# Kernel optimization log

Hardware: AMD Instinct MI355X
Metric: run time of the kernel (lower is better)

Reference implementation:

```python
import jax, jax.numpy as jnp
import numpy as np

B, S, D = 8, 1024, 1024
H = 2048            # expert hidden dim
E = 8               # num experts
TOP_K = 2
D_NOISE = 256
TEMP = 1.0


def setup_inputs() -> dict:
    key = jax.random.key(0)
    ks = jax.random.split(key, 8)
    return {
        "x": jax.random.normal(ks[0], (B, S, D), dtype=jnp.float32),
        "noise_clock_emb": jax.random.normal(ks[1], (B, D_NOISE), dtype=jnp.float32),
        # router weight [D_noise, E] (xavier-ish scale)
        "route_weight": jax.random.normal(ks[2], (D_NOISE, E), dtype=jnp.float32) * (1.0 / np.sqrt(D_NOISE)),
        # stacked expert params; torch Linear y = x @ W.T + b, stored here pre-transposed
        "fc_in_w": jax.random.normal(ks[3], (E, D, 2 * H), dtype=jnp.float32) * 0.02,
        "fc_in_b": jax.random.normal(ks[4], (E, 2 * H), dtype=jnp.float32) * 0.02,
        "fc_out_w": jax.random.normal(ks[5], (E, H, D), dtype=jnp.float32) * 0.02,
        "fc_out_b": jax.random.normal(ks[6], (E, D), dtype=jnp.float32) * 0.02,
    }


def reference(x, noise_clock_emb, route_weight, fc_in_w, fc_in_b, fc_out_w, fc_out_b):
    # ---- router: P = softmax(phi(sigma) @ W_R / T) ----
    logits = (noise_clock_emb @ route_weight) / TEMP            # [B, E]
    probs = jax.nn.softmax(logits, axis=-1)
    topk_weights, topk_indices = jax.lax.top_k(probs, TOP_K)    # [B, K]
    topk_weights = topk_weights / jnp.clip(
        topk_weights.sum(axis=-1, keepdims=True), 1e-8)
    # dense per-(batch, expert) mixing coefficient, identical to the
    # masked accumulation in the torch loop
    coeff = jnp.einsum("bke,bk->be",
                       jax.nn.one_hot(topk_indices, E, dtype=x.dtype),
                       topk_weights)                             # [B, E]

    # ---- all experts densely over the full batch (matches original math) ----
    h = jnp.einsum("bsd,edh->ebsh", x, fc_in_w) + fc_in_b[:, None, None, :]
    value, gate = jnp.split(h, 2, axis=-1)                       # [E,B,S,H] each
    hidden = value * jax.nn.silu(gate)
    mixed = jnp.einsum("ebsh,ehd,be->bsd", hidden, fc_out_w, coeff)
    mixed = mixed + jnp.einsum("be,ed->bd", coeff, fc_out_b)[:, None, :]
    return mixed, logits, probs, topk_indices, topk_weights
```

## Files before the change

kernel.cpp:

```cpp
#include <hip/hip_runtime.h>
#include <stdint.h>

#define B_ 8
#define S_ 1024
#define D_ 1024
#define H_ 2048
#define E_ 8
#define DN_ 256

typedef unsigned char u8;
typedef float f32x4 __attribute__((ext_vector_type(4)));
typedef long long ll;

__device__ __forceinline__ u8 f2f8(float f) {
  return (u8)(__builtin_amdgcn_cvt_pk_fp8_f32(f, f, 0, false) & 0xff);
}
__device__ __forceinline__ unsigned int pk4f8(float a, float b, float c, float d) {
  int w = __builtin_amdgcn_cvt_pk_fp8_f32(a, b, 0, false);
  w = __builtin_amdgcn_cvt_pk_fp8_f32(c, d, w, true);
  return (unsigned int)w;
}

__device__ __forceinline__ void gll16(const void* g, void* l) {
  __builtin_amdgcn_global_load_lds(
      (__attribute__((address_space(1))) void*)g,
      (__attribute__((address_space(3))) void*)l, 16, 0, 0);
}

__device__ __forceinline__ int swz(int r) { return (r & 3) ^ ((r >> 2) & 1); }

__global__ void router_kernel(const float* __restrict__ noise,
                              const float* __restrict__ rw,
                              float* __restrict__ out_logits,
                              float* __restrict__ out_probs,
                              float* __restrict__ out_idx,
                              float* __restrict__ out_w,
                              int* __restrict__ ws_idx,
                              float* __restrict__ ws_w) {
  __shared__ float sl[64];
  __shared__ float sp[64];
  const int t = threadIdx.x;
  const int b = t >> 3, e = t & 7;
  float acc = 0.f;
  for (int d = 0; d < DN_; ++d) acc += noise[b * DN_ + d] * rw[d * E_ + e];
  sl[t] = acc;
  out_logits[t] = acc;
  __syncthreads();
  float m = -1e30f;
  for (int j = 0; j < 8; ++j) m = fmaxf(m, sl[b * 8 + j]);
  float s = 0.f;
  for (int j = 0; j < 8; ++j) s += __expf(sl[b * 8 + j] - m);
  const float p = __expf(acc - m) / s;
  out_probs[t] = p;
  sp[t] = p;
  __syncthreads();
  if (e == 0) {
    int a1 = 0; float v1 = sp[b * 8];
    for (int j = 1; j < 8; ++j) { float v = sp[b * 8 + j]; if (v > v1) { v1 = v; a1 = j; } }
    int a2 = -1; float v2 = -1e30f;
    for (int j = 0; j < 8; ++j) {
      if (j == a1) continue;
      float v = sp[b * 8 + j]; if (v > v2) { v2 = v; a2 = j; }
    }
    float sum = fmaxf(v1 + v2, 1e-8f);
    float w1 = v1 / sum, w2 = v2 / sum;
    out_idx[b * 2] = (float)a1; out_idx[b * 2 + 1] = (float)a2;
    out_w[b * 2] = w1; out_w[b * 2 + 1] = w2;
    ws_idx[b * 2] = a1; ws_idx[b * 2 + 1] = a2;
    ws_w[b * 2] = w1; ws_w[b * 2 + 1] = w2;
  }
}

__global__ void cast_x_kernel(const float* __restrict__ x, unsigned int* __restrict__ xq) {
  const size_t i = (size_t)blockIdx.x * blockDim.x + threadIdx.x;
  float4 v = *(const float4*)(x + i * 4);
  xq[i] = pk4f8(v.x, v.y, v.z, v.w);
}

template <int R, int C>
__global__ void transpose_cast_kernel(const float* __restrict__ in, u8* __restrict__ out) {
  __shared__ u8 tile[64][72];
  const int e = blockIdx.z;
  const float* ip = in + (size_t)e * R * C;
  u8* op = out + (size_t)e * R * C;
  const int r0 = blockIdx.y * 64, c0 = blockIdx.x * 64;
  const int t = threadIdx.x;
  const int rr = t >> 4;
  const int c4 = t & 15;
#pragma unroll
  for (int i = 0; i < 4; ++i) {
    const int r = rr + i * 16;
    float4 v = *(const float4*)(ip + (size_t)(r0 + r) * C + c0 + c4 * 4);
    tile[c4 * 4 + 0][r] = f2f8(v.x);
    tile[c4 * 4 + 1][r] = f2f8(v.y);
    tile[c4 * 4 + 2][r] = f2f8(v.z);
    tile[c4 * 4 + 3][r] = f2f8(v.w);
  }
  __syncthreads();
#pragma unroll
  for (int i = 0; i < 4; ++i) {
    const int c = rr + i * 16;
    unsigned int w = *(const unsigned int*)&tile[c][c4 * 4];
    *(unsigned int*)(op + (size_t)(c0 + c) * R + r0 + c4 * 4) = w;
  }
}

__global__ void __launch_bounds__(256, 4) gemm1_kernel(
    const u8* __restrict__ xq,
    const u8* __restrict__ wtin,
    const float* __restrict__ bin,
    const int* __restrict__ ws_idx, const float* __restrict__ ws_w,
    u8* __restrict__ hid)
{
  const int nt = blockIdx.x;
  const int mt = blockIdx.y;
  const int z  = blockIdx.z;
  const int b  = z >> 1;
  const int e  = ws_idx[z] & 7;
  const float csc = ws_w[z];

  __shared__ u8 As[128 * 64];
  __shared__ u8 Bs[128 * 64];

  const int t = threadIdx.x;
  const int wave = t >> 6, lane = t & 63;
  const int wm = wave >> 1, wn = wave & 1;
  const int lm = lane & 15, lq = lane >> 4;
  const int lrow4 = lane >> 2;
  const int kq = ((lane & 3) ^ swz(lrow4)) * 16;
  const int fsw = swz(lm);
  const int p0 = lq >> 1, fb = (lq & 1) * 8;

  const u8* Ab  = xq + (size_t)b * (S_ * D_) + (size_t)mt * 128 * D_;
  const u8* Bvb = wtin + (size_t)e * (2 * H_ * D_) + (size_t)nt * 64 * D_;
  const u8* Bgb = Bvb + (size_t)H_ * D_;

  const f32x4 vz = {0.f, 0.f, 0.f, 0.f};
  f32x4 accv[4][2], accg[4][2];
#pragma unroll
  for (int i = 0; i < 4; ++i)
#pragma unroll
    for (int j = 0; j < 2; ++j) { accv[i][j] = vz; accg[i][j] = vz; }

  for (int kt = 0; kt < D_ / 64; ++kt) {
    const int k0 = kt * 64 + kq;
    gll16(Ab + (size_t)(wave * 16 + lrow4) * D_ + k0, (char*)As + wave * 1024);
    gll16(Ab + (size_t)((wave + 4) * 16 + lrow4) * D_ + k0, (char*)As + (wave + 4) * 1024);
    gll16(Bvb + (size_t)(wave * 16 + lrow4) * D_ + k0, (char*)Bs + wave * 1024);
    gll16(Bgb + (size_t)(wave * 16 + lrow4) * D_ + k0, (char*)Bs + 4096 + wave * 1024);
    __syncthreads();
    ll af[4][2], bvf[2][2], bgf[2][2];
#pragma unroll
    for (int h = 0; h < 2; ++h) {
      const int pw = ((h * 2 + p0) ^ fsw) * 16 + fb;
#pragma unroll
      for (int i = 0; i < 4; ++i)
        af[i][h] = *(const ll*)(As + (wm * 64 + i * 16 + lm) * 64 + pw);
#pragma unroll
      for (int j = 0; j < 2; ++j) {
        bvf[j][h] = *(const ll*)(Bs + (wn * 32 + j * 16 + lm) * 64 + pw);
        bgf[j][h] = *(const ll*)(Bs + (64 + wn * 32 + j * 16 + lm) * 64 + pw);
      }
    }
#pragma unroll
    for (int h = 0; h < 2; ++h)
#pragma unroll
      for (int i = 0; i < 4; ++i)
#pragma unroll
        for (int j = 0; j < 2; ++j) {
          accv[i][j] = __builtin_amdgcn_mfma_f32_16x16x32_fp8_fp8(af[i][h], bvf[j][h], accv[i][j], 0, 0, 0);
          accg[i][j] = __builtin_amdgcn_mfma_f32_16x16x32_fp8_fp8(af[i][h], bgf[j][h], accg[i][j], 0, 0, 0);
        }
    __syncthreads();
  }

  u8* hb = hid + (size_t)z * (S_ * H_);
  const int row0 = mt * 128 + wm * 64;
  const int col0 = nt * 64 + wn * 32;
#pragma unroll
  for (int j = 0; j < 2; ++j) {
    const int col = col0 + j * 16 + lm;
    const float bvx = bin[e * 2 * H_ + col];
    const float bgx = bin[e * 2 * H_ + H_ + col];
#pragma unroll
    for (int i = 0; i < 4; ++i) {
#pragma unroll
      for (int r = 0; r < 4; ++r) {
        const int srow = row0 + i * 16 + lq * 4 + r;
        float v = accv[i][j][r] + bvx;
        float g = accg[i][j][r] + bgx;
        float hv = v * g / (1.f + __expf(-g)) * csc;
        hb[(size_t)srow * H_ + col] = f2f8(hv);
      }
    }
  }
}

__global__ void __launch_bounds__(256, 2) gemm2_kernel(
    const u8* __restrict__ hid,
    const u8* __restrict__ wtout,
    const float* __restrict__ bout,
    const int* __restrict__ ws_idx, const float* __restrict__ ws_w,
    float* __restrict__ out)
{
  const int nt = blockIdx.x;
  const int mt = blockIdx.y;
  const int b  = blockIdx.z;

  __shared__ u8 As[128 * 64];
  __shared__ u8 Bs[128 * 64];

  const int t = threadIdx.x;
  const int wave = t >> 6, lane = t & 63;
  const int wm = wave >> 1, wn = wave & 1;
  const int lm = lane & 15, lq = lane >> 4;
  const int lrow4 = lane >> 2;
  const int kq = ((lane & 3) ^ swz(lrow4)) * 16;
  const int fsw = swz(lm);
  const int p0 = lq >> 1, fb = (lq & 1) * 8;

  const f32x4 vz = {0.f, 0.f, 0.f, 0.f};
  f32x4 acc[4][4];
#pragma unroll
  for (int i = 0; i < 4; ++i)
#pragma unroll
    for (int j = 0; j < 4; ++j) acc[i][j] = vz;

  for (int slot = 0; slot < 2; ++slot) {
    const int e = ws_idx[b * 2 + slot] & 7;
    const u8* Ab = hid + ((size_t)(b * 2 + slot) * S_ + mt * 128) * H_;
    const u8* Bb = wtout + ((size_t)e * D_ + nt * 128) * H_;
    for (int kt = 0; kt < H_ / 64; ++kt) {
      const int k0 = kt * 64 + kq;
      gll16(Ab + (size_t)(wave * 16 + lrow4) * H_ + k0, (char*)As + wave * 1024);
      gll16(Ab + (size_t)((wave + 4) * 16 + lrow4) * H_ + k0, (char*)As + (wave + 4) * 1024);
      gll16(Bb + (size_t)(wave * 16 + lrow4) * H_ + k0, (char*)Bs + wave * 1024);
      gll16(Bb + (size_t)((wave + 4) * 16 + lrow4) * H_ + k0, (char*)Bs + (wave + 4) * 1024);
      __syncthreads();
      ll af[4][2], bf[4][2];
#pragma unroll
      for (int h = 0; h < 2; ++h) {
        const int pw = ((h * 2 + p0) ^ fsw) * 16 + fb;
#pragma unroll
        for (int i = 0; i < 4; ++i)
          af[i][h] = *(const ll*)(As + (wm * 64 + i * 16 + lm) * 64 + pw);
#pragma unroll
        for (int j = 0; j < 4; ++j)
          bf[j][h] = *(const ll*)(Bs + (wn * 64 + j * 16 + lm) * 64 + pw);
      }
#pragma unroll
      for (int h = 0; h < 2; ++h)
#pragma unroll
        for (int i = 0; i < 4; ++i)
#pragma unroll
          for (int j = 0; j < 4; ++j)
            acc[i][j] = __builtin_amdgcn_mfma_f32_16x16x32_fp8_fp8(af[i][h], bf[j][h], acc[i][j], 0, 0, 0);
      __syncthreads();
    }
  }

  const int e0 = ws_idx[b * 2] & 7, e1 = ws_idx[b * 2 + 1] & 7;
  const float c0 = ws_w[b * 2], c1 = ws_w[b * 2 + 1];
  float* ob = out + (size_t)b * (S_ * D_);
  const int row0 = mt * 128 + wm * 64;
  const int col0 = nt * 128 + wn * 64;
#pragma unroll
  for (int j = 0; j < 4; ++j) {
    const int col = col0 + j * 16 + lm;
    const float bias = c0 * bout[e0 * D_ + col] + c1 * bout[e1 * D_ + col];
#pragma unroll
    for (int i = 0; i < 4; ++i)
#pragma unroll
      for (int r = 0; r < 4; ++r)
        ob[(size_t)(row0 + i * 16 + lq * 4 + r) * D_ + col] = acc[i][j][r] + bias;
  }
}

extern "C" void kernel_launch(void* const* d_in, const int* in_sizes, int n_in,
                              void* d_out, int out_size, void* d_ws, size_t ws_size,
                              hipStream_t stream) {
  const float* x     = (const float*)d_in[0];
  const float* noise = (const float*)d_in[1];
  const float* rw    = (const float*)d_in[2];
  const float* fiw   = (const float*)d_in[3];
  const float* fib   = (const float*)d_in[4];
  const float* fow   = (const float*)d_in[5];
  const float* fob   = (const float*)d_in[6];
  float* out = (float*)d_out;

  char* ws = (char*)d_ws;
  int*   ws_idx = (int*)ws;
  float* ws_w   = (float*)(ws + 64);
  u8* xq    = (u8*)(ws + 256);
  u8* wtin  = xq + (size_t)B_ * S_ * D_;
  u8* wtout = wtin + (size_t)E_ * 2 * H_ * D_;
  u8* hid   = wtout + (size_t)E_ * D_ * H_;

  float* out_mixed  = out;
  float* out_logits = out + (size_t)B_ * S_ * D_;
  float* out_probs  = out_logits + B_ * E_;
  float* out_idx    = out_probs + B_ * E_;
  float* out_w      = out_idx + B_ * 2;

  router_kernel<<<1, 64, 0, stream>>>(noise, rw, out_logits, out_probs,
                                      out_idx, out_w, ws_idx, ws_w);
  cast_x_kernel<<<(B_ * S_ * D_ / 4) / 256, 256, 0, stream>>>(x, (unsigned int*)xq);
  transpose_cast_kernel<D_, 2 * H_><<<dim3((2 * H_) / 64, D_ / 64, E_), 256, 0, stream>>>(fiw, wtin);
  transpose_cast_kernel<H_, D_><<<dim3(D_ / 64, H_ / 64, E_), 256, 0, stream>>>(fow, wtout);
  gemm1_kernel<<<dim3(32, 8, 16), 256, 0, stream>>>(xq, wtin, fib, ws_idx, ws_w, hid);
  gemm2_kernel<<<dim3(8, 8, 8), 256, 0, stream>>>(hid, wtout, fob, ws_idx, ws_w, out_mixed);
}
```

Baseline: 464.0 us.

## Merge router, casts and transposes into one prep kernel; halve gemm2 N tile

Folds the router, the x fp8 cast and both weight transpose-casts into a single block-indexed prep kernel, removing three launches and the gaps between them. The router now splits its dot product across four lanes with shuffle reduction. Separately, gemm2 moves to a 128x64 tile with twice as many blocks and higher launch-bounds occupancy, so more of the GPU is busy in that stage. The trade-off is that the A tile is loaded twice as often in gemm2, and the router block runs alongside the bulk cast blocks.

Result: faster. 432.0 us (-6.9%).

```diff
diff --git a/kernel.cpp b/kernel.cpp
--- a/kernel.cpp
+++ b/kernel.cpp
@@ -29,62 +29,12 @@
 
 __device__ __forceinline__ int swz(int r) { return (r & 3) ^ ((r >> 2) & 1); }
 
-__global__ void router_kernel(const float* __restrict__ noise,
-                              const float* __restrict__ rw,
-                              float* __restrict__ out_logits,
-                              float* __restrict__ out_probs,
-                              float* __restrict__ out_idx,
-                              float* __restrict__ out_w,
-                              int* __restrict__ ws_idx,
-                              float* __restrict__ ws_w) {
-  __shared__ float sl[64];
-  __shared__ float sp[64];
-  const int t = threadIdx.x;
-  const int b = t >> 3, e = t & 7;
-  float acc = 0.f;
-  for (int d = 0; d < DN_; ++d) acc += noise[b * DN_ + d] * rw[d * E_ + e];
-  sl[t] = acc;
-  out_logits[t] = acc;
-  __syncthreads();
-  float m = -1e30f;
-  for (int j = 0; j < 8; ++j) m = fmaxf(m, sl[b * 8 + j]);
-  float s = 0.f;
-  for (int j = 0; j < 8; ++j) s += __expf(sl[b * 8 + j] - m);
-  const float p = __expf(acc - m) / s;
-  out_probs[t] = p;
-  sp[t] = p;
-  __syncthreads();
-  if (e == 0) {
-    int a1 = 0; float v1 = sp[b * 8];
-    for (int j = 1; j < 8; ++j) { float v = sp[b * 8 + j]; if (v > v1) { v1 = v; a1 = j; } }
-    int a2 = -1; float v2 = -1e30f;
-    for (int j = 0; j < 8; ++j) {
-      if (j == a1) continue;
-      float v = sp[b * 8 + j]; if (v > v2) { v2 = v; a2 = j; }
-    }
-    float sum = fmaxf(v1 + v2, 1e-8f);
-    float w1 = v1 / sum, w2 = v2 / sum;
-    out_idx[b * 2] = (float)a1; out_idx[b * 2 + 1] = (float)a2;
-    out_w[b * 2] = w1; out_w[b * 2 + 1] = w2;
-    ws_idx[b * 2] = a1; ws_idx[b * 2 + 1] = a2;
-    ws_w[b * 2] = w1; ws_w[b * 2 + 1] = w2;
-  }
-}
-
-__global__ void cast_x_kernel(const float* __restrict__ x, unsigned int* __restrict__ xq) {
-  const size_t i = (size_t)blockIdx.x * blockDim.x + threadIdx.x;
-  float4 v = *(const float4*)(x + i * 4);
-  xq[i] = pk4f8(v.x, v.y, v.z, v.w);
-}
-
 template <int R, int C>
-__global__ void transpose_cast_kernel(const float* __restrict__ in, u8* __restrict__ out) {
-  __shared__ u8 tile[64][72];
-  const int e = blockIdx.z;
-  const float* ip = in + (size_t)e * R * C;
-  u8* op = out + (size_t)e * R * C;
-  const int r0 = blockIdx.y * 64, c0 = blockIdx.x * 64;
-  const int t = threadIdx.x;
+__device__ __forceinline__ void transpose_body(const float* __restrict__ ip,
+                                               u8* __restrict__ op,
+                                               int bx, int by, int t,
+                                               u8 (&tile)[64][72]) {
+  const int r0 = by * 64, c0 = bx * 64;
   const int rr = t >> 4;
   const int c4 = t & 15;
 #pragma unroll
@@ -102,6 +52,91 @@
     const int c = rr + i * 16;
     unsigned int w = *(const unsigned int*)&tile[c][c4 * 4];
     *(unsigned int*)(op + (size_t)(c0 + c) * R + r0 + c4 * 4) = w;
+  }
+}
+
+#define NCAST (B_ * S_ * D_ / 1024)
+#define NT1 ((2 * H_ / 64) * (D_ / 64) * E_)
+#define NT2 ((D_ / 64) * (H_ / 64) * E_)
+
+__global__ void __launch_bounds__(256) prep_kernel(
+    const float* __restrict__ x, const float* __restrict__ noise,
+    const float* __restrict__ rw, const float* __restrict__ fiw,
+    const float* __restrict__ fow,
+    float* __restrict__ out_logits, float* __restrict__ out_probs,
+    float* __restrict__ out_idx, float* __restrict__ out_w,
+    int* __restrict__ ws_idx, float* __restrict__ ws_w,
+    unsigned int* __restrict__ xq, u8* __restrict__ wtin,
+    u8* __restrict__ wtout) {
+  __shared__ __align__(16) u8 tile[64][72];
+  const int t = threadIdx.x;
+  int bid = blockIdx.x;
+
+  if (bid == 0) {
+    float* sl = (float*)&tile[0][0];
+    float* sp = sl + 64;
+    {
+      const int pair = t >> 2, sub = t & 3;
+      const int b = pair >> 3, e = pair & 7;
+      float acc = 0.f;
+      const int d0 = sub * 64;
+      for (int d = d0; d < d0 + 64; ++d)
+        acc += noise[b * DN_ + d] * rw[d * E_ + e];
+      acc += __shfl_xor(acc, 1);
+      acc += __shfl_xor(acc, 2);
+      if (sub == 0) sl[pair] = acc;
+    }
+    __syncthreads();
+    if (t < 64) {
+      const int b = t >> 3;
+      float L = sl[t];
+      out_logits[t] = L;
+      float m = -1e30f;
+      for (int j = 0; j < 8; ++j) m = fmaxf(m, sl[b * 8 + j]);
+      float s = 0.f;
+      for (int j = 0; j < 8; ++j) s += __expf(sl[b * 8 + j] - m);
+      float p = __expf(L - m) / s;
+      out_probs[t] = p;
+      sp[t] = p;
+    }
+    __syncthreads();
+    if (t < 64 && (t & 7) == 0) {
+      const int b = t >> 3;
+      int a1 = 0; float v1 = sp[b * 8];
+      for (int j = 1; j < 8; ++j) { float v = sp[b * 8 + j]; if (v > v1) { v1 = v; a1 = j; } }
+      int a2 = -1; float v2 = -1e30f;
+      for (int j = 0; j < 8; ++j) {
+        if (j == a1) continue;
+        float v = sp[b * 8 + j]; if (v > v2) { v2 = v; a2 = j; }
+      }
+      float sum = fmaxf(v1 + v2, 1e-8f);
+      float w1 = v1 / sum, w2 = v2 / sum;
+      out_idx[b * 2] = (float)a1; out_idx[b * 2 + 1] = (float)a2;
+      out_w[b * 2] = w1; out_w[b * 2 + 1] = w2;
+      ws_idx[b * 2] = a1; ws_idx[b * 2 + 1] = a2;
+      ws_w[b * 2] = w1; ws_w[b * 2 + 1] = w2;
+    }
+    return;
+  }
+  bid -= 1;
+  if (bid < NCAST) {
+    const size_t i = (size_t)bid * 256 + t;
+    float4 v = *((const float4*)x + i);
+    xq[i] = pk4f8(v.x, v.y, v.z, v.w);
+    return;
+  }
+  bid -= NCAST;
+  if (bid < NT1) {
+    const int bx = bid & 63, by = (bid >> 6) & 15, e = bid >> 10;
+    transpose_body<D_, 2 * H_>(fiw + (size_t)e * D_ * 2 * H_,
+                               wtin + (size_t)e * D_ * 2 * H_, bx, by, t, tile);
+    return;
+  }
+  bid -= NT1;
+  {
+    const int bx = bid & 15, by = (bid >> 4) & 31, e = bid >> 9;
+    transpose_body<H_, D_>(fow + (size_t)e * H_ * D_,
+                           wtout + (size_t)e * H_ * D_, bx, by, t, tile);
   }
 }
 
@@ -196,7 +231,7 @@
   }
 }
 
-__global__ void __launch_bounds__(256, 2) gemm2_kernel(
+__global__ void __launch_bounds__(256, 4) gemm2_kernel(
     const u8* __restrict__ hid,
     const u8* __restrict__ wtout,
     const float* __restrict__ bout,
@@ -208,7 +243,7 @@
   const int b  = blockIdx.z;
 
   __shared__ u8 As[128 * 64];
-  __shared__ u8 Bs[128 * 64];
+  __shared__ u8 Bs[64 * 64];
 
   const int t = threadIdx.x;
   const int wave = t >> 6, lane = t & 63;
@@ -220,24 +255,23 @@
   const int p0 = lq >> 1, fb = (lq & 1) * 8;
 
   const f32x4 vz = {0.f, 0.f, 0.f, 0.f};
-  f32x4 acc[4][4];
+  f32x4 acc[4][2];
 #pragma unroll
   for (int i = 0; i < 4; ++i)
 #pragma unroll
-    for (int j = 0; j < 4; ++j) acc[i][j] = vz;
+    for (int j = 0; j < 2; ++j) acc[i][j] = vz;
 
   for (int slot = 0; slot < 2; ++slot) {
     const int e = ws_idx[b * 2 + slot] & 7;
     const u8* Ab = hid + ((size_t)(b * 2 + slot) * S_ + mt * 128) * H_;
-    const u8* Bb = wtout + ((size_t)e * D_ + nt * 128) * H_;
+    const u8* Bb = wtout + ((size_t)e * D_ + nt * 64) * H_;
     for (int kt = 0; kt < H_ / 64; ++kt) {
       const int k0 = kt * 64 + kq;
       gll16(Ab + (size_t)(wave * 16 + lrow4) * H_ + k0, (char*)As + wave * 1024);
       gll16(Ab + (size_t)((wave + 4) * 16 + lrow4) * H_ + k0, (char*)As + (wave + 4) * 1024);
       gll16(Bb + (size_t)(wave * 16 + lrow4) * H_ + k0, (char*)Bs + wave * 1024);
-      gll16(Bb + (size_t)((wave + 4) * 16 + lrow4) * H_ + k0, (char*)Bs + (wave + 4) * 1024);
       __syncthreads();
-      ll af[4][2], bf[4][2];
+      ll af[4][2], bf[2][2];
 #pragma unroll
       for (int h = 0; h < 2; ++h) {
         const int pw = ((h * 2 + p0) ^ fsw) * 16 + fb;
@@ -245,15 +279,15 @@
         for (int i = 0; i < 4; ++i)
           af[i][h] = *(const ll*)(As + (wm * 64 + i * 16 + lm) * 64 + pw);
 #pragma unroll
-        for (int j = 0; j < 4; ++j)
-          bf[j][h] = *(const ll*)(Bs + (wn * 64 + j * 16 + lm) * 64 + pw);
+        for (int j = 0; j < 2; ++j)
+          bf[j][h] = *(const ll*)(Bs + (wn * 32 + j * 16 + lm) * 64 + pw);
       }
 #pragma unroll
       for (int h = 0; h < 2; ++h)
 #pragma unroll
         for (int i = 0; i < 4; ++i)
 #pragma unroll
-          for (int j = 0; j < 4; ++j)
+          for (int j = 0; j < 2; ++j)
             acc[i][j] = __builtin_amdgcn_mfma_f32_16x16x32_fp8_fp8(af[i][h], bf[j][h], acc[i][j], 0, 0, 0);
       __syncthreads();
     }
@@ -263,9 +297,9 @@
   const float c0 = ws_w[b * 2], c1 = ws_w[b * 2 + 1];
   float* ob = out + (size_t)b * (S_ * D_);
   const int row0 = mt * 128 + wm * 64;
-  const int col0 = nt * 128 + wn * 64;
-#pragma unroll
-  for (int j = 0; j < 4; ++j) {
+  const int col0 = nt * 64 + wn * 32;
+#pragma unroll
+  for (int j = 0; j < 2; ++j) {
     const int col = col0 + j * 16 + lm;
     const float bias = c0 * bout[e0 * D_ + col] + c1 * bout[e1 * D_ + col];
 #pragma unroll
@@ -302,11 +336,9 @@
   float* out_idx    = out_probs + B_ * E_;
   float* out_w      = out_idx + B_ * 2;
 
-  router_kernel<<<1, 64, 0, stream>>>(noise, rw, out_logits, out_probs,
-                                      out_idx, out_w, ws_idx, ws_w);
-  cast_x_kernel<<<(B_ * S_ * D_ / 4) / 256, 256, 0, stream>>>(x, (unsigned int*)xq);
-  transpose_cast_kernel<D_, 2 * H_><<<dim3((2 * H_) / 64, D_ / 64, E_), 256, 0, stream>>>(fiw, wtin);
-  transpose_cast_kernel<H_, D_><<<dim3(D_ / 64, H_ / 64, E_), 256, 0, stream>>>(fow, wtout);
+  prep_kernel<<<1 + NCAST + NT1 + NT2, 256, 0, stream>>>(
+      x, noise, rw, fiw, fow, out_logits, out_probs, out_idx, out_w,
+      ws_idx, ws_w, (unsigned int*)xq, wtin, wtout);
   gemm1_kernel<<<dim3(32, 8, 16), 256, 0, stream>>>(xq, wtin, fib, ws_idx, ws_w, hid);
-  gemm2_kernel<<<dim3(8, 8, 8), 256, 0, stream>>>(hid, wtout, fob, ws_idx, ws_w, out_mixed);
-}
+  gemm2_kernel<<<dim3(16, 8, 8), 256, 0, stream>>>(hid, wtout, fob, ws_idx, ws_w, out_mixed);
+}
```
